# Kernel tuning notes

Measured on AMD Instinct MI355X. Metric: run time of the kernel, lower is better.

Reference implementation:

```python
import jax, jax.numpy as jnp
import numpy as np

N, E, IN_DIM, OUT_DIM, NNZ = 4096, 2048, 256, 256, 65536
ALPHA = 0.2          # LeakyReLU negative slope
NEG_GAT = -9e15      # masked_fill value for GAT adjacency mask
NEG_ATT = -1e9       # masked_fill value inside ScaledDotProductAttention_hyper


def setup_inputs() -> dict:
    key = jax.random.key(0)
    ks = jax.random.split(key, 10)
    stdv = 1.0 / np.sqrt(OUT_DIM)
    u = lambda k, shape: jax.random.uniform(k, shape, jnp.float32, -stdv, stdv)
    x = jax.random.normal(ks[0], (N, IN_DIM), jnp.float32)
    node_idx = jax.random.randint(ks[1], (NNZ,), 0, N, jnp.int32)
    edge_idx = jax.random.randint(ks[2], (NNZ,), 0, E, jnp.int32)
    hyperedge_index = jnp.stack([node_idx, edge_idx])  # [2, NNZ]
    return {
        "x": x,
        "weight": u(ks[3], (IN_DIM, OUT_DIM)),
        "weight2": u(ks[4], (IN_DIM, OUT_DIM)),
        "weight3": u(ks[5], (OUT_DIM, OUT_DIM)),
        "weight_g": u(ks[6], (IN_DIM, OUT_DIM)),
        "a_g": u(ks[7], (2 * OUT_DIM, 1)),
        "word_context": u(ks[8], (1, OUT_DIM)),
        "bias": u(ks[9], (OUT_DIM,)),
        "hyperedge_index": hyperedge_index,
        "num_edges": E,
    }


def reference(x, weight, weight2, weight3, weight_g, a_g, word_context, bias,
              hyperedge_index, num_edges):
    n = x.shape[0]
    d = weight_g.shape[1]
    temp = d ** 0.5  # temperature = out_features ** 0.5

    # --- hypergraph preprocessing: dense incidence H [N, E] and node adjacency A [N, N]
    H = jnp.zeros((n, num_edges), x.dtype).at[hyperedge_index[0], hyperedge_index[1]].set(1.0)
    A = (H @ H.T > 0).astype(x.dtype)
    A = A.at[jnp.arange(n), jnp.arange(n)].set(1.0)  # fill_diagonal_(1)

    # --- dense GAT-style attention over the clique-expanded graph
    Wh_g = x @ weight_g                               # [N, D]
    Wh1 = Wh_g @ a_g[:d]                              # [N, 1]
    Wh2 = Wh_g @ a_g[d:]                              # [N, 1]
    e_g = jax.nn.leaky_relu(Wh1 + Wh2.T, ALPHA)       # [N, N]
    attention_g = jax.nn.softmax(jnp.where(A > 0, e_g, NEG_GAT), axis=1)

    # --- project node-node attention onto hyperedges: [N, E]
    graph2hyper = attention_g @ H

    # --- dual hypergraph cross-attention (eval mode: dropout is identity)
    x_4att = x @ weight2                              # [N, D]
    xw = x @ weight + bias                            # [N, D] (transfer=True)

    # attention1: hyperedge queries attend over nodes, mask = H.T [E, N]
    q1 = jnp.broadcast_to(word_context[0], (num_edges, d))
    attn1 = (q1 / temp) @ x_4att.T                    # [E, N]
    attn1 = jnp.where(H.T == 0, NEG_ATT, attn1)
    att1 = jax.nn.softmax(graph2hyper.T, axis=-1) + jax.nn.softmax(attn1, axis=-1)
    edge = att1 @ xw                                  # [E, D]
    att2he = att1.T                                   # [N, E]

    # attention2: node queries attend over hyperedges, mask = H [N, E]
    edge_4att = edge @ weight3                        # [E, D]
    attn2 = (x_4att / temp) @ edge_4att.T             # [N, E]
    attn2 = jnp.where(H == 0, NEG_ATT, attn2)
    att2hn = jax.nn.softmax(graph2hyper, axis=-1) + jax.nn.softmax(attn2, axis=-1)
    node = att2hn @ edge                              # [N, D]

    # --- combine attentions and aggregate
    att2_he_out = att2he @ att2he.T                   # [N, N]
    att2_hn_out = att2hn @ att2hn.T                   # [N, N]
    attention_out = attention_g + att2_he_out + att2_hn_out
    h_prime_g = jax.nn.elu(attention_out @ Wh_g)      # concat=True -> ELU

    node = jax.nn.relu(node)                          # concat=True -> ReLU, then squeeze
    return node, h_prime_g
```

## Files before the change

kernel.cpp:

```cpp
#include <hip/hip_runtime.h>
#include <cstdint>
#include <cstddef>


#define DI __device__ __forceinline__
typedef unsigned short u16;
typedef unsigned char  u8;
typedef unsigned int   u32;
typedef __bf16 bf16x8 __attribute__((ext_vector_type(8)));
typedef float  f32x4  __attribute__((ext_vector_type(4)));
typedef u32    u32x4  __attribute__((ext_vector_type(4)));
typedef int    i32x4  __attribute__((ext_vector_type(4)));
typedef int    i32x8  __attribute__((ext_vector_type(8)));

constexpr int NN  = 4096;
constexpr int EE  = 2048;
constexpr int NNZb = 65536;

constexpr size_t MB = (size_t)1 << 20;
constexpr size_t OFF_HBITS   = 0;
constexpr size_t OFF_HBITST  = 1*MB;
constexpr size_t OFF_ABITS   = 2*MB;
constexpr size_t OFF_EDGE    = 2*MB;
constexpr size_t OFF_WH1     = 4*MB;
constexpr size_t OFF_WH2     = 4*MB + 16384;
constexpr size_t OFF_V       = 4*MB + 32768;
constexpr size_t OFF_RSINV   = 4*MB + 49152;
constexpr size_t OFF_WCAT    = 5*MB;
constexpr size_t OFF_XB      = 6*MB;
constexpr size_t OFF_EDGET   = 6*MB;
constexpr size_t OFF_HN2T    = 7*MB;
constexpr size_t OFF_WHG     = 8*MB;
constexpr size_t OFF_X4ATT   = 10*MB;
constexpr size_t OFF_YB      = 12*MB;
constexpr size_t OFF_XWT     = 14*MB;
constexpr size_t OFF_WHGTA   = 16*MB;
constexpr size_t OFF_HBT     = 18*MB;
constexpr size_t OFF_EDGE2T  = 18*MB;
constexpr size_t OFF_WHGTB   = 26*MB;
constexpr size_t OFF_EXPA    = 36*MB;
constexpr size_t OFF_ATT1    = 36*MB;
constexpr size_t OFF_ATT2HN  = 36*MB;
constexpr size_t OFF_ATT1T   = 52*MB;
constexpr size_t OFF_G2H     = 68*MB;
constexpr size_t OFF_G2HT    = 84*MB;
constexpr size_t OFF_ATT2HNT = 84*MB;
constexpr size_t OFF_ATTN2   = 100*MB;
constexpr size_t OFF_G1      = 116*MB;
constexpr size_t OFF_C2      = 120*MB;
constexpr size_t OFF_HN2ACC  = 124*MB;

DI u16 to_bf(float f) {
  union { float f; u32 u; } x; x.f = f;
  u32 r = x.u + 0x7fffu + ((x.u >> 16) & 1u);
  return (u16)(r >> 16);
}
DI float from_bf(u16 h) { union { u32 u; float f; } x; x.u = (u32)h << 16; return x.f; }
DI void store_bf4(u16* p, float a, float b, float c, float d) {
  u32 lo = (u32)to_bf(a) | ((u32)to_bf(b) << 16);
  u32 hi = (u32)to_bf(c) | ((u32)to_bf(d) << 16);
  *(u32*)p = lo; *((u32*)p + 1) = hi;
}
DI u32 pack_fp8x4(float a, float b, float c, float d) {
  int p = __builtin_amdgcn_cvt_pk_fp8_f32(a, b, 0, false);
  p = __builtin_amdgcn_cvt_pk_fp8_f32(c, d, p, true);
  return (u32)p;
}

DI float wredf(float v) {
  #pragma unroll
  for (int o = 32; o; o >>= 1) v += __shfl_down(v, o);
  return v;
}
DI int wredi(int v) {
  #pragma unroll
  for (int o = 32; o; o >>= 1) v += __shfl_down(v, o);
  return v;
}

typedef __attribute__((address_space(3))) void lds_void;
typedef __attribute__((address_space(1))) void glb_void;
DI void async_load16(const void* g, void* l) {
  __builtin_amdgcn_global_load_lds((glb_void*)(uintptr_t)g,
                                   (lds_void*)(u32)(uintptr_t)l, 16, 0, 0);
}

template <int BM, int BN, class Epi>
DI void gemm_body(const u16* __restrict__ A, const u16* __restrict__ B,
                  int nb, int K, int k0, int kLen, Epi epi, int tile,
                  u16* As, u16* Bs)
{
  constexpr int BK = 64;
  constexpr int WM = BM / 2, WN = BN / 2;
  constexpr int FM = WM / 16, FN = WN / 16;
  constexpr int AI = (BM * 8) / 256, BI = (BN * 8) / 256;

  const int tid = threadIdx.x;
  const int w = tid >> 6, l = tid & 63;
  const int bi = tile / nb, bj = tile - bi * nb;
  const int i0 = bi * BM, j0 = bj * BN;
  const int wm = (w & 1) * WM, wn = (w >> 1) * WN;
  const int quad = l >> 4, m16 = l & 15;

  f32x4 acc[FM][FN] = {};

  for (int kb = k0; kb < k0 + kLen; kb += BK) {
    __syncthreads();
    #pragma unroll
    for (int i = 0; i < AI; ++i) {
      const int ci = (i * 4 + w) * 64 + l;
      const int r = ci >> 3;
      const int lc = (ci & 7) ^ (r & 7);
      async_load16(A + (size_t)(i0 + r) * K + kb + lc * 8, &As[(i * 4 + w) * 512]);
    }
    #pragma unroll
    for (int i = 0; i < BI; ++i) {
      const int ci = (i * 4 + w) * 64 + l;
      const int r = ci >> 3;
      const int lc = (ci & 7) ^ (r & 7);
      async_load16(B + (size_t)(j0 + r) * K + kb + lc * 8, &Bs[(i * 4 + w) * 512]);
    }
    __syncthreads();
    #pragma unroll
    for (int ks = 0; ks < 2; ++ks) {
      bf16x8 af[FM], bfv[FN];
      #pragma unroll
      for (int mi = 0; mi < FM; ++mi) {
        const int row = wm + mi * 16 + m16;
        af[mi] = *(const bf16x8*)&As[row * BK + (((ks * 4 + quad) ^ (row & 7)) * 8)];
      }
      #pragma unroll
      for (int ni = 0; ni < FN; ++ni) {
        const int row = wn + ni * 16 + m16;
        bfv[ni] = *(const bf16x8*)&Bs[row * BK + (((ks * 4 + quad) ^ (row & 7)) * 8)];
      }
      #pragma unroll
      for (int mi = 0; mi < FM; ++mi)
        #pragma unroll
        for (int ni = 0; ni < FN; ++ni)
          acc[mi][ni] = __builtin_amdgcn_mfma_f32_16x16x32_bf16(
              af[mi], bfv[ni], acc[mi][ni], 0, 0, 0);
    }
  }
  #pragma unroll
  for (int mi = 0; mi < FM; ++mi)
    #pragma unroll
    for (int ni = 0; ni < FN; ++ni) {
      const int rb = i0 + wm + mi * 16 + quad * 4;
      const int c  = j0 + wn + ni * 16 + m16;
      epi(rb, c, acc[mi][ni]);
    }
}

DI void t32_tile(const u16* __restrict__ in, u16* __restrict__ out,
                 int R, int C, int bx, int by, u16* t) {
  int tx = threadIdx.x & 31, ty = threadIdx.x >> 5;
  int x0 = bx * 32, y0 = by * 32;
  #pragma unroll
  for (int k = 0; k < 32; k += 8)
    t[(ty + k) * 33 + tx] = in[(size_t)(y0 + ty + k) * C + x0 + tx];
  __syncthreads();
  #pragma unroll
  for (int k = 0; k < 32; k += 8)
    out[(size_t)(x0 + ty + k) * R + y0 + tx] = t[tx * 33 + ty + k];
}

struct EpiG0 {
  u16 *whg, *whgTa, *x4, *xwT; u8* whgTb; const float* bias;
  DI void operator()(int r, int c, f32x4 v) const {
    if (c < 256) {
      #pragma unroll
      for (int i = 0; i < 4; ++i) whg[(r + i) * 256 + c] = to_bf(v[i]);
      store_bf4(&whgTa[(size_t)c * NN + r], v[0], v[1], v[2], v[3]);
      *(u32*)&whgTb[(size_t)c * NN + r] = pack_fp8x4(v[0], v[1], v[2], v[3]);
    } else if (c < 512) {
      #pragma unroll
      for (int i = 0; i < 4; ++i) x4[(r + i) * 256 + (c - 256)] = to_bf(v[i]);
    } else {
      float b = bias[c - 512];
      store_bf4(&xwT[(size_t)(c - 512) * NN + r], v[0]+b, v[1]+b, v[2]+b, v[3]+b);
    }
  }
};
struct EpiBig {
  const float* rsInv; u16* g2h; u16* g2hT; float* g1;
  DI void operator()(int r, int c, f32x4 v) const {
    float w0 = v[0]*rsInv[r], w1 = v[1]*rsInv[r+1], w2 = v[2]*rsInv[r+2], w3 = v[3]*rsInv[r+3];
    if (c < 2048) {
      g2h[(size_t)r * EE + c] = to_bf(w0);
      g2h[(size_t)(r+1) * EE + c] = to_bf(w1);
      g2h[(size_t)(r+2) * EE + c] = to_bf(w2);
      g2h[(size_t)(r+3) * EE + c] = to_bf(w3);
      store_bf4(&g2hT[(size_t)c * NN + r], w0, w1, w2, w3);
    } else {
      g1[(r) * 256 + (c - 2048)] = w0;
      g1[(r+1) * 256 + (c - 2048)] = w1;
      g1[(r+2) * 256 + (c - 2048)] = w2;
      g1[(r+3) * 256 + (c - 2048)] = w3;
    }
  }
};
struct EpiEdgeT {
  u16 *edgeT, *edge2T, *edge;
  DI void operator()(int r, int c, f32x4 v) const {
    if (r < 256) {
      #pragma unroll
      for (int i = 0; i < 4; ++i) edgeT[(size_t)(r + i) * EE + c] = to_bf(v[i]);
      store_bf4(&edge[(size_t)c * 256 + r], v[0], v[1], v[2], v[3]);
    } else {
      #pragma unroll
      for (int i = 0; i < 4; ++i) edge2T[(size_t)(r - 256 + i) * EE + c] = to_bf(v[i]);
    }
  }
};
struct EpiCombine {
  const float* g1; const float* c2; float* out;
  DI void operator()(int r, int c, f32x4 v) const {
    if (c < 256) {
      #pragma unroll
      for (int i = 0; i < 4; ++i) out[(r + i) * 256 + c] = fmaxf(v[i], 0.f);
    } else {
      int d = c - 256;
      #pragma unroll
      for (int i = 0; i < 4; ++i) {
        float s = g1[(r + i) * 256 + d] + c2[(r + i) * 256 + d] + v[i];
        out[1048576 + (r + i) * 256 + d] = s > 0.f ? s : expm1f(s);
      }
    }
  }
};
struct EpiBf16 { u16* out; int ldn;
  DI void operator()(int r, int c, f32x4 v) const {
    #pragma unroll
    for (int i = 0; i < 4; ++i) out[(size_t)(r + i) * ldn + c] = to_bf(v[i]);
  } };
struct EpiBf16Scale { u16* out; int ldn; float s;
  DI void operator()(int r, int c, f32x4 v) const {
    #pragma unroll
    for (int i = 0; i < 4; ++i) out[(size_t)(r + i) * ldn + c] = to_bf(v[i] * s);
  } };
struct EpiF32 { float* out; int ldn;
  DI void operator()(int r, int c, f32x4 v) const {
    #pragma unroll
    for (int i = 0; i < 4; ++i) out[(size_t)(r + i) * ldn + c] = v[i];
  } };
struct EpiAtomF32 { float* out; int ldn;
  DI void operator()(int r, int c, f32x4 v) const {
    #pragma unroll
    for (int i = 0; i < 4; ++i) atomicAdd(&out[(size_t)(r + i) * ldn + c], v[i]);
  } };

template <int BM, int BN, int S, int LB, class Epi>
__global__ __launch_bounds__(256, LB)
void gemm_k(const u16* __restrict__ A, const u16* __restrict__ B,
            int nb, int K, Epi epi) {
  __shared__ __align__(16) u16 smem[(BM + BN) * 64];
  int t = blockIdx.x;
  int k0 = 0, kLen = K;
  if (S > 1) {
    const int tilesPer = gridDim.x / S;
    const int s = t / tilesPer; t -= s * tilesPer;
    kLen = K / S; k0 = s * kLen;
  }
  gemm_body<BM, BN>(A, B, nb, K, k0, kLen, epi, t, smem, smem + BM * 64);
}

template <class Epi>
__global__ __launch_bounds__(256, 3)
void gemm_mx(const u8* __restrict__ A, const u8* __restrict__ B,
             int nb, int K, Epi epi) {
  constexpr int BM = 128, BN = 96, BK = 128;
  constexpr int FM = 4, FN = 3;
  __shared__ __align__(16) u8 As[BM * BK];
  __shared__ __align__(16) u8 Bs[BN * BK];

  const int tid = threadIdx.x;
  const int w = tid >> 6, l = tid & 63;
  const int tile = blockIdx.x;
  const int bi = tile / nb, bj = tile - bi * nb;
  const int i0 = bi * BM, j0 = bj * BN;
  const int wm = (w & 1) * 64, wn = (w >> 1) * 48;
  const int quad = l >> 4, m16 = l & 15;

  f32x4 acc[FM][FN] = {};

  for (int kb = 0; kb < K; kb += BK) {
    __syncthreads();
    #pragma unroll
    for (int i = 0; i < 4; ++i) {
      const int ci = (i * 4 + w) * 64 + l;
      const int r = ci >> 3;
      const int lc = (ci & 7) ^ (r & 7);
      async_load16(A + (size_t)(i0 + r) * K + kb + lc * 16, &As[(i * 4 + w) * 1024]);
    }
    #pragma unroll
    for (int i = 0; i < 3; ++i) {
      const int ci = (i * 4 + w) * 64 + l;
      const int r = ci >> 3;
      const int lc = (ci & 7) ^ (r & 7);
      async_load16(B + (size_t)(j0 + r) * K + kb + lc * 16, &Bs[(i * 4 + w) * 1024]);
    }
    __syncthreads();
    i32x8 af[FM], bf[FN];
    #pragma unroll
    for (int mi = 0; mi < FM; ++mi) {
      const int row = wm + mi * 16 + m16;
      const i32x4 lo = *(const i32x4*)&As[row * BK + ((quad * 2) ^ (row & 7)) * 16];
      const i32x4 hi = *(const i32x4*)&As[row * BK + ((quad * 2 + 1) ^ (row & 7)) * 16];
      af[mi][0] = lo[0]; af[mi][1] = lo[1]; af[mi][2] = lo[2]; af[mi][3] = lo[3];
      af[mi][4] = hi[0]; af[mi][5] = hi[1]; af[mi][6] = hi[2]; af[mi][7] = hi[3];
    }
    #pragma unroll
    for (int ni = 0; ni < FN; ++ni) {
      const int row = wn + ni * 16 + m16;
      const i32x4 lo = *(const i32x4*)&Bs[row * BK + ((quad * 2) ^ (row & 7)) * 16];
      const i32x4 hi = *(const i32x4*)&Bs[row * BK + ((quad * 2 + 1) ^ (row & 7)) * 16];
      bf[ni][0] = lo[0]; bf[ni][1] = lo[1]; bf[ni][2] = lo[2]; bf[ni][3] = lo[3];
      bf[ni][4] = hi[0]; bf[ni][5] = hi[1]; bf[ni][6] = hi[2]; bf[ni][7] = hi[3];
    }
    #pragma unroll
    for (int mi = 0; mi < FM; ++mi)
      #pragma unroll
      for (int ni = 0; ni < FN; ++ni)
        acc[mi][ni] = __builtin_amdgcn_mfma_scale_f32_16x16x128_f8f6f4(
            af[mi], bf[ni], acc[mi][ni], 0, 0,
            0, 0x7F7F7F7F, 0, 0x7F7F7F7F);
  }
  #pragma unroll
  for (int mi = 0; mi < FM; ++mi)
    #pragma unroll
    for (int ni = 0; ni < FN; ++ni) {
      const int rb = i0 + wm + mi * 16 + quad * 4;
      const int c  = j0 + wn + ni * 16 + m16;
      epi(rb, c, acc[mi][ni]);
    }
}

__global__ void k_prep(const float* wg, const float* w2, const float* w1,
                       const float* w3, const float* x, u16* wcat, u16* xb,
                       char* zbits, char* zhbt, char* zhn2) {
  int idx = blockIdx.x * 256 + threadIdx.x;
  if (blockIdx.x < 5120) {
    if (idx < 196608) {
      int blk = idx >> 16, r = idx & 65535;
      int d = r >> 8, kk = r & 255;
      const float* src = blk == 0 ? wg : blk == 1 ? w2 : w1;
      wcat[idx] = to_bf(src[kk * 256 + d]);
    } else if (idx < 262144) {
      int r = idx - 196608;
      wcat[196608 + r] = to_bf(w3[r]);
    } else {
      int r = idx - 262144;
      xb[r] = to_bf(x[r]);
    }
  } else {
    int z = idx - 5120 * 256;
    u32x4 zero = {0, 0, 0, 0};
    if (z < 262144)      ((u32x4*)zbits)[z] = zero;
    else if (z < 786432) ((u32x4*)zhbt)[z - 262144] = zero;
    else                 ((u32x4*)zhn2)[z - 786432] = zero;
  }
}

__global__ void k_scatter_diag(const int* __restrict__ hidx, u32* hbits, u32* hbitsT,
                               u8* hbT, u32* abits) {
  int k = blockIdx.x * 256 + threadIdx.x;
  if (k < NNZb) {
    int n = hidx[k], e = hidx[NNZb + k];
    atomicOr(&hbits[n * 64 + (e >> 5)], 1u << (e & 31));
    atomicOr(&hbitsT[e * 128 + (n >> 5)], 1u << (n & 31));
    hbT[(size_t)e * NN + n] = 0x38;
  } else {
    int i = k - NNZb;
    if (i < NN) atomicOr(&abits[i * 128 + (i >> 5)], 1u << (i & 31));
  }
}

__global__ void k_rowclique(const u16* __restrict__ whg, const u16* __restrict__ x4,
                            const float* __restrict__ ag, const float* __restrict__ wc,
                            float* wh1, float* wh2, float* v,
                            const u32* __restrict__ hbitsT, u32* abits) {
  __shared__ int list[512];
  __shared__ int cnt;
  int tid = threadIdx.x;
  if (blockIdx.x < 1024) {
    int wv = tid >> 6, l = tid & 63;
    int row = blockIdx.x * 4 + wv;
    float s1 = 0, s2 = 0, s3 = 0;
    #pragma unroll
    for (int dd = 0; dd < 4; ++dd) {
      int d = l * 4 + dd;
      float a = from_bf(whg[row * 256 + d]);
      s1 += a * ag[d]; s2 += a * ag[256 + d];
      s3 += from_bf(x4[row * 256 + d]) * wc[d];
    }
    s1 = wredf(s1); s2 = wredf(s2); s3 = wredf(s3);
    if (l == 0) { wh1[row] = s1; wh2[row] = s2; v[row] = s3 * (1.0f / 16.0f); }
  } else {
    int e = blockIdx.x - 1024;
    if (tid == 0) cnt = 0;
    __syncthreads();
    if (tid < 128) {
      u32 w = hbitsT[e * 128 + tid];
      while (w) {
        int b = __ffs(w) - 1;
        int p = atomicAdd(&cnt, 1);
        if (p < 512) list[p] = tid * 32 + b;
        w &= w - 1;
      }
    }
    __syncthreads();
    int c = cnt < 512 ? cnt : 512;
    for (int p = tid; p < c * c; p += 256) {
      int i = list[p / c], j = list[p % c];
      atomicOr(&abits[i * 128 + (j >> 5)], 1u << (j & 31));
    }
  }
}

__global__ void k_exprows(const u32* __restrict__ abits, const float* __restrict__ wh1,
                          const float* __restrict__ wh2, u8* __restrict__ expA,
                          float* rsInv) {
  int i = blockIdx.x, tid = threadIdx.x;
  __shared__ float ssum;
  if (tid == 0) ssum = 0.f;
  __syncthreads();
  float a = wh1[i], lsum = 0.f;
  #pragma unroll
  for (int it = 0; it < 4; ++it) {
    int j = it * 1024 + tid * 4;
    u32 w = abits[i * 128 + (j >> 5)];
    u32 m = (w >> (j & 31)) & 0xFu;
    const f32x4 wv = *(const f32x4*)&wh2[j];
    float x0 = 0.f, x1 = 0.f, x2 = 0.f, x3 = 0.f;
    if (m & 1u) { float z = a + wv[0]; float eg = z > 0.f ? z : 0.2f * z; x0 = __expf(eg); }
    if (m & 2u) { float z = a + wv[1]; float eg = z > 0.f ? z : 0.2f * z; x1 = __expf(eg); }
    if (m & 4u) { float z = a + wv[2]; float eg = z > 0.f ? z : 0.2f * z; x2 = __expf(eg); }
    if (m & 8u) { float z = a + wv[3]; float eg = z > 0.f ? z : 0.2f * z; x3 = __expf(eg); }
    u32 word = pack_fp8x4(x0, x1, x2, x3);
    *(u32*)&expA[(size_t)i * NN + j] = word;
    lsum += __builtin_amdgcn_cvt_f32_fp8(word, 0) + __builtin_amdgcn_cvt_f32_fp8(word, 1)
          + __builtin_amdgcn_cvt_f32_fp8(word, 2) + __builtin_amdgcn_cvt_f32_fp8(word, 3);
  }
  lsum = wredf(lsum);
  if ((tid & 63) == 0) atomicAdd(&ssum, lsum);
  __syncthreads();
  if (tid == 0) rsInv[i] = 1.0f / ssum;
}

__global__ void k_edge_softmax(const u16* __restrict__ g2hT, const u32* __restrict__ hbitsT,
                               const float* __restrict__ v, u16* __restrict__ att1) {
  int e = blockIdx.x, tid = threadIdx.x;
  __shared__ float evals[NN];
  __shared__ u32 hw[128];
  __shared__ float s1s, s2s; __shared__ int cs;
  if (tid == 0) { s1s = 0.f; s2s = 0.f; cs = 0; }
  if (tid < 128) hw[tid] = hbitsT[e * 128 + tid];
  __syncthreads();
  float sum1 = 0.f;
  for (int j = tid; j < NN; j += 256) {
    float ev = __expf(from_bf(g2hT[(size_t)e * NN + j]));
    evals[j] = ev; sum1 += ev;
  }
  float sum2 = 0.f; int cnt = 0;
  if (tid < 128) {
    u32 w = hw[tid]; cnt = __popc(w);
    while (w) { int b = __ffs(w) - 1; sum2 += __expf(v[tid * 32 + b]); w &= w - 1; }
  }
  sum1 = wredf(sum1); sum2 = wredf(sum2); cnt = wredi(cnt);
  if ((tid & 63) == 0) { atomicAdd(&s1s, sum1); atomicAdd(&s2s, sum2); atomicAdd(&cs, cnt); }
  __syncthreads();
  float inv1 = 1.0f / s1s;
  int c = cs;
  float inv2 = c > 0 ? 1.0f / s2s : 0.0f;
  float unif = c > 0 ? 0.0f : (1.0f / (float)NN);
  for (int j = tid; j < NN; j += 256) {
    float t = evals[j] * inv1 + unif;
    if ((hw[j >> 5] >> (j & 31)) & 1) t += __expf(v[j]) * inv2;
    att1[(size_t)e * NN + j] = to_bf(t);
  }
}

__global__ __launch_bounds__(256, 2)
void k_tri_edge(const u16* __restrict__ Fcat, const u16* __restrict__ Att1,
                EpiEdgeT e0,
                const u16* __restrict__ X4att, const u16* __restrict__ W3b,
                EpiBf16 e1,
                const u16* __restrict__ tin, u16* __restrict__ tout) {
  __shared__ __align__(16) u16 smem[192 * 64];
  int b = blockIdx.x;
  if (b < 256) {
    const int xcd = b & 7, idx = b >> 3;
    const int t = (idx / 4) * 32 + xcd * 4 + (idx & 3);
    gemm_body<64, 64>(Fcat, Att1, 32, NN, 0, NN, e0, t, smem, smem + 64 * 64);
  }
  else if (b < 384) gemm_body<128, 64>(X4att, W3b, 4, 256, 0, 256, e1, b - 256, smem, smem + 128 * 64);
  else { int t = b - 384; t32_tile(tin, tout, EE, NN, t & 127, t >> 7, smem); }
}

__global__ __launch_bounds__(256, 2)
void k_dual_attn2(const u16* __restrict__ Att1T, const u16* __restrict__ Edge2T,
                  EpiF32 e0,
                  const u16* __restrict__ Yb, const u16* __restrict__ Edge,
                  EpiBf16Scale e1) {
  __shared__ __align__(16) u16 smem[256 * 64];
  int b = blockIdx.x;
  if (b < 128) gemm_body<128, 64>(Att1T, Edge2T, 4, EE, 0, EE, e0, b, smem, smem + 128 * 64);
  else         gemm_body<128, 128>(Yb, Edge, 16, 256, 0, 256, e1, b - 128, smem, smem + 128 * 64);
}

__global__ void k_node_softmax(const u16* __restrict__ g2h, const u16* __restrict__ attn2,
                               const u32* __restrict__ hbits, u16* __restrict__ att2hn) {
  int n = blockIdx.x, tid = threadIdx.x;
  __shared__ float ev3[EE], ev4[EE];
  __shared__ u32 hw[64];
  __shared__ float s3s, s4s; __shared__ int cs;
  if (tid == 0) { s3s = 0.f; s4s = 0.f; cs = 0; }
  if (tid < 64) hw[tid] = hbits[n * 64 + tid];
  __syncthreads();
  float s3 = 0.f, s4 = 0.f; int cl = 0;
  for (int e = tid; e < EE; e += 256) {
    float x3 = __expf(from_bf(g2h[(size_t)n * EE + e]));
    ev3[e] = x3; s3 += x3;
    bool m = (hw[e >> 5] >> (e & 31)) & 1;
    float x4 = m ? __expf(from_bf(attn2[(size_t)n * EE + e])) : 0.f;
    ev4[e] = x4; s4 += x4; cl += m;
  }
  s3 = wredf(s3); s4 = wredf(s4); cl = wredi(cl);
  if ((tid & 63) == 0) { atomicAdd(&s3s, s3); atomicAdd(&s4s, s4); atomicAdd(&cs, cl); }
  __syncthreads();
  float inv3 = 1.0f / s3s;
  int c = cs;
  float inv4 = c > 0 ? 1.0f / s4s : 0.0f;
  float unif = c > 0 ? 0.0f : (1.0f / (float)EE);
  for (int e = tid; e < EE; e += 256)
    att2hn[(size_t)n * EE + e] = to_bf(ev3[e] * inv3 + ev4[e] * inv4 + unif);
}

__global__ void k_transpose(const u16* __restrict__ in, u16* __restrict__ out,
                            int R, int C) {
  __shared__ u16 t[32 * 33];
  t32_tile(in, out, R, C, blockIdx.x, blockIdx.y, t);
}

__global__ void k_cast_hn2(const float* __restrict__ acc, u16* __restrict__ hn2T) {
  int idx = blockIdx.x * 256 + threadIdx.x;
  hn2T[idx] = to_bf(acc[idx]);
}

extern "C" void kernel_launch(void* const* d_in, const int* in_sizes, int n_in,
                              void* d_out, int out_size, void* d_ws, size_t ws_size,
                              hipStream_t stream) {
  (void)in_sizes; (void)n_in; (void)out_size; (void)ws_size;
  const float* x    = (const float*)d_in[0];
  const float* w1   = (const float*)d_in[1];
  const float* w2   = (const float*)d_in[2];
  const float* w3   = (const float*)d_in[3];
  const float* wg   = (const float*)d_in[4];
  const float* ag   = (const float*)d_in[5];
  const float* wc   = (const float*)d_in[6];
  const float* bias = (const float*)d_in[7];
  const int*   hidx = (const int*)d_in[8];
  float* out = (float*)d_out;
  char* ws = (char*)d_ws;

  u32* Hbits   = (u32*)(ws + OFF_HBITS);
  u32* HbitsT  = (u32*)(ws + OFF_HBITST);
  u32* Abits   = (u32*)(ws + OFF_ABITS);
  float* Wh1   = (float*)(ws + OFF_WH1);
  float* Wh2   = (float*)(ws + OFF_WH2);
  float* V     = (float*)(ws + OFF_V);
  float* RsInv = (float*)(ws + OFF_RSINV);
  u16* Wcat    = (u16*)(ws + OFF_WCAT);
  u16* W3b     = Wcat + 196608;
  u16* Xb      = (u16*)(ws + OFF_XB);
  u16* Whg     = (u16*)(ws + OFF_WHG);
  u16* X4att   = (u16*)(ws + OFF_X4ATT);
  u16* Yb      = (u16*)(ws + OFF_YB);
  u16* XwT     = (u16*)(ws + OFF_XWT);
  u16* WhgTa   = (u16*)(ws + OFF_WHGTA);
  u8*  HbT8    = (u8*)(ws + OFF_HBT);
  u8*  WhgTb8  = (u8*)(ws + OFF_WHGTB);
  u8*  ExpA8   = (u8*)(ws + OFF_EXPA);
  u16* Att1    = (u16*)(ws + OFF_ATT1);
  u16* Att1T   = (u16*)(ws + OFF_ATT1T);
  u16* Att2hn  = (u16*)(ws + OFF_ATT2HN);
  u16* G2h     = (u16*)(ws + OFF_G2H);
  u16* G2hT    = (u16*)(ws + OFF_G2HT);
  u16* Att2hnT = (u16*)(ws + OFF_ATT2HNT);
  u16* Attn2   = (u16*)(ws + OFF_ATTN2);
  float* G1    = (float*)(ws + OFF_G1);
  float* C2    = (float*)(ws + OFF_C2);
  float* Hn2Acc = (float*)(ws + OFF_HN2ACC);
  u16* Edge    = (u16*)(ws + OFF_EDGE);
  u16* EdgeT   = (u16*)(ws + OFF_EDGET);
  u16* Hn2T    = (u16*)(ws + OFF_HN2T);
  u16* Edge2T  = (u16*)(ws + OFF_EDGE2T);

  k_prep<<<8704, 256, 0, stream>>>(wg, w2, w1, w3, x, Wcat, Xb,
                                   ws + OFF_HBITS, ws + OFF_HBT, ws + OFF_HN2ACC);
  k_scatter_diag<<<272, 256, 0, stream>>>(hidx, Hbits, HbitsT, HbT8, Abits);
  gemm_k<128, 64, 1, 3><<<384, 256, 0, stream>>>(
      Xb, Wcat, 12, 256, EpiG0{Whg, WhgTa, X4att, XwT, WhgTb8, bias});
  k_rowclique<<<3072, 256, 0, stream>>>(Whg, X4att, ag, wc, Wh1, Wh2, V,
                                        HbitsT, Abits);
  k_exprows<<<NN, 256, 0, stream>>>(Abits, Wh1, Wh2, ExpA8, RsInv);
  gemm_mx<<<768, 256, 0, stream>>>(
      ExpA8, HbT8, 24, NN, EpiBig{RsInv, G2h, G2hT, G1});
  k_edge_softmax<<<EE, 256, 0, stream>>>(G2hT, HbitsT, V, Att1);
  k_tri_edge<<<8576, 256, 0, stream>>>(
      XwT, Att1, EpiEdgeT{EdgeT, Edge2T, Edge},
      X4att, W3b, EpiBf16{Yb, 256},
      Att1, Att1T);
  k_dual_attn2<<<640, 256, 0, stream>>>(
      Att1T, Edge2T, EpiF32{C2, 256},
      Yb, Edge, EpiBf16Scale{Attn2, EE, 1.0f / 16.0f});
  k_node_softmax<<<NN, 256, 0, stream>>>(G2h, Attn2, Hbits, Att2hn);
  k_transpose<<<dim3(64, 128), 256, 0, stream>>>(Att2hn, Att2hnT, NN, EE);
  gemm_k<64, 64, 4, 3><<<512, 256, 0, stream>>>(
      WhgTa, Att2hnT, 32, NN, EpiAtomF32{Hn2Acc, EE});
  k_cast_hn2<<<2048, 256, 0, stream>>>(Hn2Acc, Hn2T);
  gemm_k<64, 64, 1, 2><<<512, 256, 0, stream>>>(
      Att2hn, EdgeT, 8, EE, EpiCombine{G1, C2, out});
}
```

Before: 338.3 us.

## Split-K low-occupancy GEMMs with atomics and stage transposed stores through LDS

The edge GEMM and the C2 GEMM become split-K (4 slices) with fp32 atomic accumulation into zeroed buffers, plus a new cast kernel that produces the bf16 edge/edgeT/edge2T layouts. The big fp8 GEMM epilogue now writes its transposed g2hT output through shared memory so the global stores are coalesced. The relu node GEMM is folded into the transpose kernel launch, and the final combine GEMM only computes the ELU half. The aim is more blocks for grids that were too small to fill the GPU, and fewer strided writes, at the cost of atomic traffic, extra zeroing, and one extra cast kernel.

```diff
diff --git a/kernel.cpp b/kernel.cpp
--- a/kernel.cpp
+++ b/kernel.cpp
@@ -45,6 +45,7 @@
 constexpr size_t OFF_G2H     = 68*MB;
 constexpr size_t OFF_G2HT    = 84*MB;
 constexpr size_t OFF_ATT2HNT = 84*MB;
+constexpr size_t OFF_EDGEACC = 100*MB;
 constexpr size_t OFF_ATTN2   = 100*MB;
 constexpr size_t OFF_G1      = 116*MB;
 constexpr size_t OFF_C2      = 120*MB;
@@ -182,53 +183,6 @@
     }
   }
 };
-struct EpiBig {
-  const float* rsInv; u16* g2h; u16* g2hT; float* g1;
-  DI void operator()(int r, int c, f32x4 v) const {
-    float w0 = v[0]*rsInv[r], w1 = v[1]*rsInv[r+1], w2 = v[2]*rsInv[r+2], w3 = v[3]*rsInv[r+3];
-    if (c < 2048) {
-      g2h[(size_t)r * EE + c] = to_bf(w0);
-      g2h[(size_t)(r+1) * EE + c] = to_bf(w1);
-      g2h[(size_t)(r+2) * EE + c] = to_bf(w2);
-      g2h[(size_t)(r+3) * EE + c] = to_bf(w3);
-      store_bf4(&g2hT[(size_t)c * NN + r], w0, w1, w2, w3);
-    } else {
-      g1[(r) * 256 + (c - 2048)] = w0;
-      g1[(r+1) * 256 + (c - 2048)] = w1;
-      g1[(r+2) * 256 + (c - 2048)] = w2;
-      g1[(r+3) * 256 + (c - 2048)] = w3;
-    }
-  }
-};
-struct EpiEdgeT {
-  u16 *edgeT, *edge2T, *edge;
-  DI void operator()(int r, int c, f32x4 v) const {
-    if (r < 256) {
-      #pragma unroll
-      for (int i = 0; i < 4; ++i) edgeT[(size_t)(r + i) * EE + c] = to_bf(v[i]);
-      store_bf4(&edge[(size_t)c * 256 + r], v[0], v[1], v[2], v[3]);
-    } else {
-      #pragma unroll
-      for (int i = 0; i < 4; ++i) edge2T[(size_t)(r - 256 + i) * EE + c] = to_bf(v[i]);
-    }
-  }
-};
-struct EpiCombine {
-  const float* g1; const float* c2; float* out;
-  DI void operator()(int r, int c, f32x4 v) const {
-    if (c < 256) {
-      #pragma unroll
-      for (int i = 0; i < 4; ++i) out[(r + i) * 256 + c] = fmaxf(v[i], 0.f);
-    } else {
-      int d = c - 256;
-      #pragma unroll
-      for (int i = 0; i < 4; ++i) {
-        float s = g1[(r + i) * 256 + d] + c2[(r + i) * 256 + d] + v[i];
-        out[1048576 + (r + i) * 256 + d] = s > 0.f ? s : expm1f(s);
-      }
-    }
-  }
-};
 struct EpiBf16 { u16* out; int ldn;
   DI void operator()(int r, int c, f32x4 v) const {
     #pragma unroll
@@ -239,15 +193,24 @@
     #pragma unroll
     for (int i = 0; i < 4; ++i) out[(size_t)(r + i) * ldn + c] = to_bf(v[i] * s);
   } };
-struct EpiF32 { float* out; int ldn;
-  DI void operator()(int r, int c, f32x4 v) const {
-    #pragma unroll
-    for (int i = 0; i < 4; ++i) out[(size_t)(r + i) * ldn + c] = v[i];
-  } };
 struct EpiAtomF32 { float* out; int ldn;
   DI void operator()(int r, int c, f32x4 v) const {
     #pragma unroll
     for (int i = 0; i < 4; ++i) atomicAdd(&out[(size_t)(r + i) * ldn + c], v[i]);
+  } };
+struct EpiRelu { float* out;
+  DI void operator()(int r, int c, f32x4 v) const {
+    #pragma unroll
+    for (int i = 0; i < 4; ++i) out[(r + i) * 256 + c] = fmaxf(v[i], 0.f);
+  } };
+struct EpiElu {
+  const float* g1; const float* c2; float* out;
+  DI void operator()(int r, int c, f32x4 v) const {
+    #pragma unroll
+    for (int i = 0; i < 4; ++i) {
+      float s = g1[(r + i) * 256 + c] + c2[(r + i) * 256 + c] + v[i];
+      out[1048576 + (r + i) * 256 + c] = s > 0.f ? s : expm1f(s);
+    }
   } };
 
 template <int BM, int BN, int S, int LB, class Epi>
@@ -265,14 +228,16 @@
   gemm_body<BM, BN>(A, B, nb, K, k0, kLen, epi, t, smem, smem + BM * 64);
 }
 
-template <class Epi>
 __global__ __launch_bounds__(256, 3)
 void gemm_mx(const u8* __restrict__ A, const u8* __restrict__ B,
-             int nb, int K, Epi epi) {
+             int nb, int K, const float* __restrict__ rsInv,
+             u16* __restrict__ g2h, u16* __restrict__ g2hT,
+             float* __restrict__ g1) {
   constexpr int BM = 128, BN = 96, BK = 128;
   constexpr int FM = 4, FN = 3;
-  __shared__ __align__(16) u8 As[BM * BK];
-  __shared__ __align__(16) u8 Bs[BN * BK];
+  __shared__ __align__(16) u8 smem[28672];
+  u8* As = smem;
+  u8* Bs = smem + BM * BK;
 
   const int tid = threadIdx.x;
   const int w = tid >> 6, l = tid & 63;
@@ -326,19 +291,37 @@
             af[mi], bf[ni], acc[mi][ni], 0, 0,
             0, 0x7F7F7F7F, 0, 0x7F7F7F7F);
   }
+  const int ncol = j0 < 2048 ? ((2048 - j0) < BN ? (2048 - j0) : BN) : 0;
+  u16* T2 = (u16*)smem;
+  __syncthreads();
   #pragma unroll
   for (int mi = 0; mi < FM; ++mi)
     #pragma unroll
     for (int ni = 0; ni < FN; ++ni) {
-      const int rb = i0 + wm + mi * 16 + quad * 4;
-      const int c  = j0 + wn + ni * 16 + m16;
-      epi(rb, c, acc[mi][ni]);
-    }
+      const int rb = wm + mi * 16 + quad * 4;
+      const int cl = wn + ni * 16 + m16;
+      const int gc = j0 + cl;
+      #pragma unroll
+      for (int rg = 0; rg < 4; ++rg) {
+        float sv = acc[mi][ni][rg] * rsInv[i0 + rb + rg];
+        if (gc < 2048) {
+          u16 hv = to_bf(sv);
+          g2h[(size_t)(i0 + rb + rg) * EE + gc] = hv;
+          T2[cl * 130 + rb + rg] = hv;
+        } else {
+          g1[(i0 + rb + rg) * 256 + (gc - 2048)] = sv;
+        }
+      }
+    }
+  __syncthreads();
+  const u32* T2d = (const u32*)T2;
+  for (int c = w; c < ncol; c += 4)
+    *(u32*)&g2hT[(size_t)(j0 + c) * NN + i0 + 2 * l] = T2d[c * 65 + l];
 }
 
 __global__ void k_prep(const float* wg, const float* w2, const float* w1,
                        const float* w3, const float* x, u16* wcat, u16* xb,
-                       char* zbits, char* zhbt, char* zhn2) {
+                       char* zbits, char* zhbt, char* zhn2, char* zc2) {
   int idx = blockIdx.x * 256 + threadIdx.x;
   if (blockIdx.x < 5120) {
     if (idx < 196608) {
@@ -356,9 +339,10 @@
   } else {
     int z = idx - 5120 * 256;
     u32x4 zero = {0, 0, 0, 0};
-    if (z < 262144)      ((u32x4*)zbits)[z] = zero;
-    else if (z < 786432) ((u32x4*)zhbt)[z - 262144] = zero;
-    else                 ((u32x4*)zhn2)[z - 786432] = zero;
+    if (z < 262144)       ((u32x4*)zbits)[z] = zero;
+    else if (z < 786432)  ((u32x4*)zhbt)[z - 262144] = zero;
+    else if (z < 917504)  ((u32x4*)zhn2)[z - 786432] = zero;
+    else                  ((u32x4*)zc2)[z - 917504] = zero;
   }
 }
 
@@ -449,11 +433,13 @@
 }
 
 __global__ void k_edge_softmax(const u16* __restrict__ g2hT, const u32* __restrict__ hbitsT,
-                               const float* __restrict__ v, u16* __restrict__ att1) {
+                               const float* __restrict__ v, u16* __restrict__ att1,
+                               float* __restrict__ edgeAcc) {
   int e = blockIdx.x, tid = threadIdx.x;
   __shared__ float evals[NN];
   __shared__ u32 hw[128];
   __shared__ float s1s, s2s; __shared__ int cs;
+  if (tid < 128) ((f32x4*)(edgeAcc))[(size_t)e * 128 + tid] = f32x4{0.f, 0.f, 0.f, 0.f};
   if (tid == 0) { s1s = 0.f; s2s = 0.f; cs = 0; }
   if (tid < 128) hw[tid] = hbitsT[e * 128 + tid];
   __syncthreads();
@@ -483,30 +469,57 @@
 
 __global__ __launch_bounds__(256, 2)
 void k_tri_edge(const u16* __restrict__ Fcat, const u16* __restrict__ Att1,
-                EpiEdgeT e0,
+                EpiAtomF32 e0,
                 const u16* __restrict__ X4att, const u16* __restrict__ W3b,
                 EpiBf16 e1,
                 const u16* __restrict__ tin, u16* __restrict__ tout) {
   __shared__ __align__(16) u16 smem[192 * 64];
   int b = blockIdx.x;
-  if (b < 256) {
-    const int xcd = b & 7, idx = b >> 3;
-    const int t = (idx / 4) * 32 + xcd * 4 + (idx & 3);
-    gemm_body<64, 64>(Fcat, Att1, 32, NN, 0, NN, e0, t, smem, smem + 64 * 64);
-  }
-  else if (b < 384) gemm_body<128, 64>(X4att, W3b, 4, 256, 0, 256, e1, b - 256, smem, smem + 128 * 64);
-  else { int t = b - 384; t32_tile(tin, tout, EE, NN, t & 127, t >> 7, smem); }
+  if (b < 1024) {
+    const int s = b >> 8, t = b & 255;
+    gemm_body<64, 64>(Fcat, Att1, 32, NN, s * 1024, 1024, e0, t, smem, smem + 64 * 64);
+  }
+  else if (b < 1152) gemm_body<128, 64>(X4att, W3b, 4, 256, 0, 256, e1, b - 1024, smem, smem + 128 * 64);
+  else { int t = b - 1152; t32_tile(tin, tout, EE, NN, t & 127, t >> 7, smem); }
+}
+
+__global__ void k_cast_edge(const float* __restrict__ acc, u16* __restrict__ edgeT,
+                            u16* __restrict__ edge2T, u16* __restrict__ edge) {
+  int b = blockIdx.x, tid = threadIdx.x;
+  if (b < 1024) {
+    int base = (b * 256 + tid) * 4;
+    f32x4 v = *(const f32x4*)&acc[base];
+    int row = base >> 11, col = base & 2047;
+    u16* dst = row < 256 ? &edgeT[row * 2048 + col] : &edge2T[(row - 256) * 2048 + col];
+    store_bf4(dst, v[0], v[1], v[2], v[3]);
+  } else {
+    __shared__ float t[32 * 33];
+    int b2 = b - 1024;
+    int by = b2 >> 6, bx = b2 & 63;
+    int tx = tid & 31, ty = tid >> 5;
+    #pragma unroll
+    for (int k = 0; k < 32; k += 8)
+      t[(ty + k) * 33 + tx] = acc[(size_t)(by * 32 + ty + k) * 2048 + bx * 32 + tx];
+    __syncthreads();
+    #pragma unroll
+    for (int k = 0; k < 32; k += 8)
+      edge[(size_t)(bx * 32 + ty + k) * 256 + by * 32 + tx] = to_bf(t[tx * 33 + ty + k]);
+  }
 }
 
 __global__ __launch_bounds__(256, 2)
 void k_dual_attn2(const u16* __restrict__ Att1T, const u16* __restrict__ Edge2T,
-                  EpiF32 e0,
+                  EpiAtomF32 e0,
                   const u16* __restrict__ Yb, const u16* __restrict__ Edge,
                   EpiBf16Scale e1) {
   __shared__ __align__(16) u16 smem[256 * 64];
   int b = blockIdx.x;
-  if (b < 128) gemm_body<128, 64>(Att1T, Edge2T, 4, EE, 0, EE, e0, b, smem, smem + 128 * 64);
-  else         gemm_body<128, 128>(Yb, Edge, 16, 256, 0, 256, e1, b - 128, smem, smem + 128 * 64);
+  if (b < 512) {
+    const int s = b >> 7, t = b & 127;
+    gemm_body<128, 64>(Att1T, Edge2T, 4, EE, s * 512, 512, e0, t, smem, smem + 128 * 64);
+  } else {
+    gemm_body<128, 128>(Yb, Edge, 16, 256, 0, 256, e1, b - 512, smem, smem + 128 * 64);
+  }
 }
 
 __global__ void k_node_softmax(const u16* __restrict__ g2h, const u16* __restrict__ attn2,
@@ -537,10 +550,15 @@
     att2hn[(size_t)n * EE + e] = to_bf(ev3[e] * inv3 + ev4[e] * inv4 + unif);
 }
 
-__global__ void k_transpose(const u16* __restrict__ in, u16* __restrict__ out,
-                            int R, int C) {
-  __shared__ u16 t[32 * 33];
-  t32_tile(in, out, R, C, blockIdx.x, blockIdx.y, t);
+__global__ __launch_bounds__(256, 2)
+void k_dual_t_c1a(const u16* __restrict__ tin, u16* __restrict__ tout,
+                  const u16* __restrict__ Att2hn, const u16* __restrict__ EdgeT,
+                  EpiRelu e1) {
+  __shared__ __align__(16) u16 smem[128 * 64];
+  int b = blockIdx.x;
+  if (b < 8192) t32_tile(tin, tout, NN, EE, b & 63, b >> 6, smem);
+  else          gemm_body<64, 64>(Att2hn, EdgeT, 4, EE, 0, EE, e1, b - 8192,
+                                  smem, smem + 64 * 64);
 }
 
 __global__ void k_cast_hn2(const float* __restrict__ acc, u16* __restrict__ hn2T) {
@@ -589,6 +607,7 @@
   u16* G2hT    = (u16*)(ws + OFF_G2HT);
   u16* Att2hnT = (u16*)(ws + OFF_ATT2HNT);
   u16* Attn2   = (u16*)(ws + OFF_ATTN2);
+  float* EdgeAcc = (float*)(ws + OFF_EDGEACC);
   float* G1    = (float*)(ws + OFF_G1);
   float* C2    = (float*)(ws + OFF_C2);
   float* Hn2Acc = (float*)(ws + OFF_HN2ACC);
@@ -597,29 +616,31 @@
   u16* Hn2T    = (u16*)(ws + OFF_HN2T);
   u16* Edge2T  = (u16*)(ws + OFF_EDGE2T);
 
-  k_prep<<<8704, 256, 0, stream>>>(wg, w2, w1, w3, x, Wcat, Xb,
-                                   ws + OFF_HBITS, ws + OFF_HBT, ws + OFF_HN2ACC);
+  k_prep<<<9728, 256, 0, stream>>>(wg, w2, w1, w3, x, Wcat, Xb,
+                                   ws + OFF_HBITS, ws + OFF_HBT,
+                                   ws + OFF_HN2ACC, ws + OFF_C2);
   k_scatter_diag<<<272, 256, 0, stream>>>(hidx, Hbits, HbitsT, HbT8, Abits);
   gemm_k<128, 64, 1, 3><<<384, 256, 0, stream>>>(
       Xb, Wcat, 12, 256, EpiG0{Whg, WhgTa, X4att, XwT, WhgTb8, bias});
   k_rowclique<<<3072, 256, 0, stream>>>(Whg, X4att, ag, wc, Wh1, Wh2, V,
                                         HbitsT, Abits);
   k_exprows<<<NN, 256, 0, stream>>>(Abits, Wh1, Wh2, ExpA8, RsInv);
-  gemm_mx<<<768, 256, 0, stream>>>(
-      ExpA8, HbT8, 24, NN, EpiBig{RsInv, G2h, G2hT, G1});
-  k_edge_softmax<<<EE, 256, 0, stream>>>(G2hT, HbitsT, V, Att1);
-  k_tri_edge<<<8576, 256, 0, stream>>>(
-      XwT, Att1, EpiEdgeT{EdgeT, Edge2T, Edge},
+  gemm_mx<<<768, 256, 0, stream>>>(ExpA8, HbT8, 24, NN, RsInv, G2h, G2hT, G1);
+  k_edge_softmax<<<EE, 256, 0, stream>>>(G2hT, HbitsT, V, Att1, EdgeAcc);
+  k_tri_edge<<<9344, 256, 0, stream>>>(
+      XwT, Att1, EpiAtomF32{EdgeAcc, 2048},
       X4att, W3b, EpiBf16{Yb, 256},
       Att1, Att1T);
-  k_dual_attn2<<<640, 256, 0, stream>>>(
-      Att1T, Edge2T, EpiF32{C2, 256},
+  k_cast_edge<<<1536, 256, 0, stream>>>(EdgeAcc, EdgeT, Edge2T, Edge);
+  k_dual_attn2<<<1024, 256, 0, stream>>>(
+      Att1T, Edge2T, EpiAtomF32{C2, 256},
       Yb, Edge, EpiBf16Scale{Attn2, EE, 1.0f / 16.0f});
   k_node_softmax<<<NN, 256, 0, stream>>>(G2h, Attn2, Hbits, Att2hn);
-  k_transpose<<<dim3(64, 128), 256, 0, stream>>>(Att2hn, Att2hnT, NN, EE);
+  k_dual_t_c1a<<<8448, 256, 0, stream>>>(Att2hn, Att2hnT,
+                                         Att2hn, EdgeT, EpiRelu{out});
   gemm_k<64, 64, 4, 3><<<512, 256, 0, stream>>>(
       WhgTa, Att2hnT, 32, NN, EpiAtomF32{Hn2Acc, EE});
   k_cast_hn2<<<2048, 256, 0, stream>>>(Hn2Acc, Hn2T);
-  gemm_k<64, 64, 1, 2><<<512, 256, 0, stream>>>(
-      Att2hn, EdgeT, 8, EE, EpiCombine{G1, C2, out});
-}
+  gemm_k<64, 64, 1, 2><<<256, 256, 0, stream>>>(
+      Att2hn, Hn2T, 4, EE, EpiElu{G1, C2, out});
+}
```

Result: slower. 354.1 us (+4.7%).
